# Performance work log

Hardware: AMD Instinct MI355X
Metric: run time of the kernel (lower is better)

Reference implementation:

```python
import jax, jax.numpy as jnp
import numpy as np

D_MODEL = 768
N_HEADS_CFG = 12
D_STATE = 32
D_CONV = 4
EXPAND = 2
HEADDIM = D_MODEL // N_HEADS_CFG          # 64
D_INNER = EXPAND * D_MODEL                # 1536
NHEADS = D_INNER // HEADDIM               # 24 (Mamba2 internal heads)
CONV_DIM = D_INNER + 2 * D_STATE          # 1600
D_IN_PROJ = 2 * D_INNER + 2 * D_STATE + NHEADS  # 3160
EPS = 1e-5
B_SZ, SEQ = 2, 512


def rmsnorm(x, w):
    return x * jax.lax.rsqrt(jnp.mean(x * x, axis=-1, keepdims=True) + EPS) * w


def mamba2(u, Wi, cw, cb, dtb, Alog, Dp, nw, Wo):
    """Mamba2 mixer: in_proj -> causal depthwise conv(silu) -> selective scan -> gated RMSNorm -> out_proj."""
    b, l, _ = u.shape
    zxbcdt = u @ Wi.T                                   # [b,l,d_in_proj]
    z, xBC, dt = jnp.split(zxbcdt, [D_INNER, D_INNER + CONV_DIM], axis=-1)
    # causal depthwise conv over time
    xBC = jnp.transpose(xBC, (0, 2, 1))                 # [b,c,l]
    xBC = jax.lax.conv_general_dilated(
        xBC, cw[:, None, :], window_strides=(1,),
        padding=[(D_CONV - 1, 0)], feature_group_count=CONV_DIM)
    xBC = jax.nn.silu(jnp.transpose(xBC + cb[None, :, None], (0, 2, 1)))
    x, Bm, Cm = jnp.split(xBC, [D_INNER, D_INNER + D_STATE], axis=-1)
    x = x.reshape(b, l, NHEADS, HEADDIM)                # [b,l,h,p]
    dt = jax.nn.softplus(dt + dtb)                      # [b,l,h]
    A = -jnp.exp(Alog)                                  # [h]
    a = jnp.exp(dt * A)                                 # decay [b,l,h]
    # dt * x outer B  -> [b,l,h,p,n]
    dBx = (dt[..., None, None] * x[..., None]) * Bm[:, :, None, None, :]

    def combine(e1, e2):
        a1, h1 = e1
        a2, h2 = e2
        return (a1 * a2, a2[..., None, None] * h1 + h2)

    _, h = jax.lax.associative_scan(combine, (a, dBx), axis=1)  # h: [b,l,h,p,n]
    y = jnp.einsum('blhpn,bln->blhp', h, Cm) + Dp[None, None, :, None] * x
    y = y.reshape(b, l, D_INNER)
    y = rmsnorm(y * jax.nn.silu(z), nw)                 # gated RMSNorm
    return y @ Wo.T                                     # [b,l,d_model]


def _mamba_params(key, scale=0.02):
    ks = jax.random.split(key, 6)
    return dict(
        in_w=jax.random.normal(ks[0], (D_IN_PROJ, D_MODEL), jnp.float32) * scale,
        conv_w=jax.random.normal(ks[1], (CONV_DIM, D_CONV), jnp.float32) * scale,
        conv_b=jnp.zeros((CONV_DIM,), jnp.float32),
        dt_bias=jax.random.uniform(ks[2], (NHEADS,), jnp.float32, -4.0, -1.0),
        A_log=jnp.log(jax.random.uniform(ks[3], (NHEADS,), jnp.float32, 1.0, 16.0)),
        D=jnp.ones((NHEADS,), jnp.float32),
        norm_w=jnp.ones((D_INNER,), jnp.float32),
        out_w=jax.random.normal(ks[4], (D_MODEL, D_INNER), jnp.float32) * scale,
    )


def setup_inputs() -> dict:
    key = jax.random.key(0)
    kx, kf, kb, ko = jax.random.split(key, 4)
    f = _mamba_params(kf)
    bw = _mamba_params(kb)
    return {
        'x': jax.random.normal(kx, (B_SZ, SEQ, D_MODEL), jnp.float32),
        'norm_w': jnp.ones((D_MODEL,), jnp.float32),
        'fwd_in_w': f['in_w'], 'fwd_conv_w': f['conv_w'], 'fwd_conv_b': f['conv_b'],
        'fwd_dt_bias': f['dt_bias'], 'fwd_A_log': f['A_log'], 'fwd_D': f['D'],
        'fwd_norm_w': f['norm_w'], 'fwd_out_w': f['out_w'],
        'bwd_in_w': bw['in_w'], 'bwd_conv_w': bw['conv_w'], 'bwd_conv_b': bw['conv_b'],
        'bwd_dt_bias': bw['dt_bias'], 'bwd_A_log': bw['A_log'], 'bwd_D': bw['D'],
        'bwd_norm_w': bw['norm_w'], 'bwd_out_w': bw['out_w'],
        'out_proj_w': jax.random.normal(ko, (D_MODEL, 2 * D_MODEL), jnp.float32) * 0.02,
    }


def reference(x, norm_w,
              fwd_in_w, fwd_conv_w, fwd_conv_b, fwd_dt_bias, fwd_A_log, fwd_D, fwd_norm_w, fwd_out_w,
              bwd_in_w, bwd_conv_w, bwd_conv_b, bwd_dt_bias, bwd_A_log, bwd_D, bwd_norm_w, bwd_out_w,
              out_proj_w):
    h = rmsnorm(x, norm_w)
    f_out = mamba2(h, fwd_in_w, fwd_conv_w, fwd_conv_b, fwd_dt_bias, fwd_A_log, fwd_D, fwd_norm_w, fwd_out_w)
    b_out = mamba2(h[:, ::-1], bwd_in_w, bwd_conv_w, bwd_conv_b, bwd_dt_bias, bwd_A_log, bwd_D, bwd_norm_w, bwd_out_w)[:, ::-1]
    return x + jnp.concatenate([f_out, b_out], axis=-1) @ out_proj_w.T
```

## Files before the change

kernel.cpp:

```cpp
#include <hip/hip_runtime.h>
#include <hip/hip_bf16.h>

#define DMODEL 768
#define DINNER 1536
#define DSTATE 32
#define NHEADS 24
#define HEADDIM 64
#define CONVDIM 1600
#define DINPROJ 3160
#define NPAD 3200
#define SEQ 512
#define MROWS 1024
#define CL 64
#define NCH 8

typedef __attribute__((ext_vector_type(8))) short bf16x8;
typedef __attribute__((ext_vector_type(4))) float f32x4;

__device__ __forceinline__ ushort f2bs(float v) {
  __hip_bfloat16 b = __float2bfloat16(v);
  return __builtin_bit_cast(unsigned short, b);
}

__device__ __forceinline__ void gld16(const void* g, const void* l) {
  __builtin_amdgcn_global_load_lds((const __attribute__((address_space(1))) void*)g,
                                   (__attribute__((address_space(3))) void*)l, 16, 0, 0);
}

__device__ __forceinline__ float block_reduce_sum(float v, float* ws4) {
#pragma unroll
  for (int o = 32; o > 0; o >>= 1) v += __shfl_xor(v, o, 64);
  int wid = threadIdx.x >> 6;
  if ((threadIdx.x & 63) == 0) ws4[wid] = v;
  __syncthreads();
  return ws4[0] + ws4[1] + ws4[2] + ws4[3];
}

__global__ __launch_bounds__(256) void prep_kernel(
    const float* __restrict__ x, const float* __restrict__ w, ushort* __restrict__ h,
    const float* __restrict__ s0, const float* __restrict__ s1,
    const float* __restrict__ s2, const float* __restrict__ s3,
    const float* __restrict__ s4, ushort* __restrict__ d) {
  if (blockIdx.x < MROWS) {
    __shared__ float ws4[4];
    int m = blockIdx.x;
    const float* xr = x + (size_t)m * DMODEL;
    float v[3];
    float ss = 0.f;
#pragma unroll
    for (int i = 0; i < 3; ++i) {
      v[i] = xr[threadIdx.x + i * 256];
      ss += v[i] * v[i];
    }
    ss = block_reduce_sum(ss, ws4);
    float sc = rsqrtf(ss / (float)DMODEL + 1e-5f);
    ushort* hr = h + (size_t)m * DMODEL;
#pragma unroll
    for (int i = 0; i < 3; ++i) {
      int c = threadIdx.x + i * 256;
      hr[c] = f2bs(v[i] * sc * w[c]);
    }
    return;
  }
  constexpr size_t NP_IN = (size_t)NPAD * DMODEL;
  constexpr size_t NE_IN = (size_t)DINPROJ * DMODEL;
  constexpr size_t NE_O = (size_t)DMODEL * DINNER;
  size_t i = (((size_t)blockIdx.x - MROWS) * 256 + threadIdx.x) * 4;
  const float* src;
  size_t off, ne;
  if (i < NP_IN) { src = s0; off = i; ne = NE_IN; }
  else if (i < 2 * NP_IN) { src = s1; off = i - NP_IN; ne = NE_IN; }
  else if (i < 2 * NP_IN + NE_O) { src = s2; off = i - 2 * NP_IN; ne = NE_O; }
  else if (i < 2 * NP_IN + 2 * NE_O) { src = s3; off = i - 2 * NP_IN - NE_O; ne = NE_O; }
  else if (i < 2 * NP_IN + 3 * NE_O) { src = s4; off = i - 2 * NP_IN - 2 * NE_O; ne = NE_O; }
  else return;
  ushort* dp = d + i;
  if (off + 3 < ne) {
    float4 v = *(const float4*)(src + off);
    dp[0] = f2bs(v.x); dp[1] = f2bs(v.y); dp[2] = f2bs(v.z); dp[3] = f2bs(v.w);
  } else {
#pragma unroll
    for (int j = 0; j < 4; ++j) dp[j] = (off + j < ne) ? f2bs(src[off + j]) : (ushort)0;
  }
}

template <int BM, int BN, bool ADD_X, bool OUT_BF16>
__global__ __launch_bounds__(256) void gemm4(
    const ushort* __restrict__ A, int lda, size_t aZ,
    const ushort* __restrict__ Bw, int ldb, size_t bZ,
    void* __restrict__ Cout, int ldc, size_t cZ,
    const float* __restrict__ X, int ldx, int K) {
  constexpr int AG = BM / 16;
  constexpr int BG = BN / 16;
  constexpr int MR = BM / 32;
  constexpr int NR = BN / 32;
  __shared__ ushort As[2][BM * 32];
  __shared__ ushort Bs[2][BN * 32];
  const int t = threadIdx.x, w = t >> 6, l = t & 63;
  int bx, by;
  {
    int gx = gridDim.x, gy = gridDim.y;
    int nwg = gx * gy;
    int flat = blockIdx.y * gx + blockIdx.x;
    int s = (flat & 7) * (nwg >> 3) + (flat >> 3);
    bx = s / gy; by = s % gy;
  }
  const int m0 = by * BM, n0 = bx * BN;
  const int wr = w >> 1, wc = w & 1;
  const int fr = l & 15, fq = l >> 4;
  const int sr = l >> 2, sc2 = (l & 3) * 8;
  const ushort* Ap = A + (size_t)blockIdx.z * aZ;
  const ushort* Bp = Bw + (size_t)blockIdx.z * bZ;

  auto stage = [&](int bb, int k0) {
#pragma unroll
    for (int g = w; g < AG + BG; g += 4) {
      if (g < AG)
        gld16(Ap + (size_t)(m0 + g * 16 + sr) * lda + k0 + sc2, (const char*)&As[bb][0] + g * 1024);
      else
        gld16(Bp + (size_t)(n0 + (g - AG) * 16 + sr) * ldb + k0 + sc2,
              (const char*)&Bs[bb][0] + (g - AG) * 1024);
    }
  };

  f32x4 acc[MR][NR];
#pragma unroll
  for (int m = 0; m < MR; ++m)
#pragma unroll
    for (int n = 0; n < NR; ++n) acc[m][n] = (f32x4){0.f, 0.f, 0.f, 0.f};

  stage(0, 0);
  __syncthreads();
  int cur = 0;
  const int nk = K / 32;
  for (int k = 0; k < nk; ++k) {
    if (k + 1 < nk) stage(cur ^ 1, (k + 1) * 32);
    bf16x8 af[MR], bfr[NR];
#pragma unroll
    for (int m = 0; m < MR; ++m)
      af[m] = *(const bf16x8*)&As[cur][(wr * (BM / 2) + m * 16 + fr) * 32 + fq * 8];
#pragma unroll
    for (int n = 0; n < NR; ++n)
      bfr[n] = *(const bf16x8*)&Bs[cur][(wc * (BN / 2) + n * 16 + fr) * 32 + fq * 8];
#pragma unroll
    for (int m = 0; m < MR; ++m)
#pragma unroll
      for (int n = 0; n < NR; ++n)
        acc[m][n] = __builtin_amdgcn_mfma_f32_16x16x32_bf16(af[m], bfr[n], acc[m][n], 0, 0, 0);
    __syncthreads();
    cur ^= 1;
  }

#pragma unroll
  for (int m = 0; m < MR; ++m) {
#pragma unroll
    for (int n = 0; n < NR; ++n) {
      int col = n0 + wc * (BN / 2) + n * 16 + fr;
#pragma unroll
      for (int j = 0; j < 4; ++j) {
        int row = m0 + wr * (BM / 2) + m * 16 + fq * 4 + j;
        float v = acc[m][n][j];
        if (ADD_X) v += X[(size_t)row * ldx + col];
        if (OUT_BF16)
          ((ushort*)Cout + (size_t)blockIdx.z * cZ)[(size_t)row * ldc + col] = f2bs(v);
        else
          ((float*)Cout + (size_t)blockIdx.z * cZ)[(size_t)row * ldc + col] = v;
      }
    }
  }
}

__global__ __launch_bounds__(256) void conv_dt_kernel(
    const float* __restrict__ zx,
    const float* __restrict__ cw0, const float* __restrict__ cb0,
    const float* __restrict__ dtb0, const float* __restrict__ Al0,
    const float* __restrict__ cw1, const float* __restrict__ cb1,
    const float* __restrict__ dtb1, const float* __restrict__ Al1,
    float* __restrict__ xbc, float* __restrict__ dta) {
  int m = blockIdx.x;
  int dir = blockIdx.y;
  int l = m & (SEQ - 1);
  const float* cw = dir ? cw1 : cw0;
  const float* cb = dir ? cb1 : cb0;
  const float* zrow = zx + (size_t)m * 6400 + dir * 3200 + DINNER;
  float* xo = xbc + ((size_t)dir * MROWS + m) * CONVDIM;
  for (int c = threadIdx.x; c < CONVDIM; c += 256) {
    float acc = cb[c];
    if (dir == 0) {
#pragma unroll
      for (int d = 0; d < 4; ++d) {
        if (l - d >= 0) acc = fmaf(zrow[-(size_t)d * 6400 + c], cw[c * 4 + 3 - d], acc);
      }
    } else {
#pragma unroll
      for (int d = 0; d < 4; ++d) {
        if (l + d < SEQ) acc = fmaf(zrow[(size_t)d * 6400 + c], cw[c * 4 + 3 - d], acc);
      }
    }
    xo[c] = acc / (1.f + expf(-acc));
  }
  if (threadIdx.x < NHEADS) {
    int hh = threadIdx.x;
    const float* dtb = dir ? dtb1 : dtb0;
    const float* Al = dir ? Al1 : Al0;
    float v = zx[(size_t)m * 6400 + dir * 3200 + DINNER + CONVDIM + hh] + dtb[hh];
    float dt = (v > 20.f) ? v : log1pf(expf(v));
    float A = -expf(Al[hh]);
    dta[((size_t)dir * MROWS + m) * 48 + hh] = dt;
    dta[((size_t)dir * MROWS + m) * 48 + NHEADS + hh] = expf(dt * A);
  }
}

__global__ __launch_bounds__(256) void scan_phase1(
    const float* __restrict__ xbc, const float* __restrict__ dta,
    float* __restrict__ sbuf, float* __restrict__ abuf) {
  __shared__ float xs[CL][64];
  __shared__ float bcs[CL][64];
  __shared__ float das[CL][2];
  int c = blockIdx.x, bh = blockIdx.y, dir = blockIdx.z;
  int b = bh / NHEADS, h = bh % NHEADS;
  int t = threadIdx.x, p = t >> 2, q = t & 3;
  const float* xb = xbc + ((size_t)dir * MROWS + b * SEQ) * CONVDIM;
  int lrow = t >> 4, lcol = (t & 15) * 4;
#pragma unroll
  for (int r = 0; r < 4; ++r) {
    int s = r * 16 + lrow;
    int tau = c * CL + s;
    int prow = dir ? (SEQ - 1 - tau) : tau;
    const float* rowp = xb + (size_t)prow * CONVDIM;
    *(float4*)&xs[s][lcol] = *(const float4*)(rowp + h * HEADDIM + lcol);
    *(float4*)&bcs[s][lcol] = *(const float4*)(rowp + DINNER + lcol);
  }
  if (t < 128) {
    int s = t >> 1, wsel = t & 1;
    int tau = c * CL + s;
    int prow = dir ? (SEQ - 1 - tau) : tau;
    das[s][wsel] = dta[((size_t)dir * MROWS + b * SEQ + prow) * 48 + wsel * NHEADS + h];
  }
  __syncthreads();
  float hst[8];
#pragma unroll
  for (int j = 0; j < 8; ++j) hst[j] = 0.f;
  float alpha = 1.f;
#pragma unroll 8
  for (int s = 0; s < CL; ++s) {
    float xp = xs[s][p];
    float dt_s = das[s][0], a_s = das[s][1];
    float cx = dt_s * xp;
    alpha *= a_s;
    float4 B0 = *(const float4*)&bcs[s][q * 8];
    float4 B1 = *(const float4*)&bcs[s][q * 8 + 4];
    float Bv[8] = {B0.x, B0.y, B0.z, B0.w, B1.x, B1.y, B1.z, B1.w};
#pragma unroll
    for (int j = 0; j < 8; ++j) hst[j] = fmaf(a_s, hst[j], cx * Bv[j]);
  }
  float* sp = sbuf + (((size_t)(dir * 48 + bh)) * NCH + c) * 2048 + p * 32 + q * 8;
  *(float4*)sp = (float4){hst[0], hst[1], hst[2], hst[3]};
  *(float4*)(sp + 4) = (float4){hst[4], hst[5], hst[6], hst[7]};
  if (t == 0) abuf[(dir * 48 + bh) * NCH + c] = alpha;
}

__global__ __launch_bounds__(256) void scan_phase3b(
    const float* __restrict__ xbc, const float* __restrict__ dta,
    const float* __restrict__ sbuf, const float* __restrict__ abuf,
    const float* __restrict__ Dp0, const float* __restrict__ Dp1,
    float* __restrict__ y) {
  __shared__ float xs[CL][64];
  __shared__ float bcs[CL][64];
  __shared__ float das[CL][2];
  int c = blockIdx.x, bh = blockIdx.y, dir = blockIdx.z;
  int b = bh / NHEADS, h = bh % NHEADS;
  int t = threadIdx.x, p = t >> 2, q = t & 3;
  const float* xb = xbc + ((size_t)dir * MROWS + b * SEQ) * CONVDIM;
  int lrow = t >> 4, lcol = (t & 15) * 4;
#pragma unroll
  for (int r = 0; r < 4; ++r) {
    int s = r * 16 + lrow;
    int tau = c * CL + s;
    int prow = dir ? (SEQ - 1 - tau) : tau;
    const float* rowp = xb + (size_t)prow * CONVDIM;
    *(float4*)&xs[s][lcol] = *(const float4*)(rowp + h * HEADDIM + lcol);
    *(float4*)&bcs[s][lcol] = *(const float4*)(rowp + DINNER + lcol);
  }
  if (t < 128) {
    int s = t >> 1, wsel = t & 1;
    int tau = c * CL + s;
    int prow = dir ? (SEQ - 1 - tau) : tau;
    das[s][wsel] = dta[((size_t)dir * MROWS + b * SEQ + prow) * 48 + wsel * NHEADS + h];
  }

  float hst[8];
#pragma unroll
  for (int j = 0; j < 8; ++j) hst[j] = 0.f;
  for (int cc = 0; cc < c; ++cc) {
    const float* sp = sbuf + (((size_t)(dir * 48 + bh)) * NCH + cc) * 2048 + p * 32 + q * 8;
    float4 s0 = *(const float4*)sp;
    float4 s1 = *(const float4*)(sp + 4);
    float al = abuf[(dir * 48 + bh) * NCH + cc];
    float sv[8] = {s0.x, s0.y, s0.z, s0.w, s1.x, s1.y, s1.z, s1.w};
#pragma unroll
    for (int j = 0; j < 8; ++j) hst[j] = fmaf(al, hst[j], sv[j]);
  }

  float Dv = (dir ? Dp1 : Dp0)[h];
  __syncthreads();
#pragma unroll 8
  for (int s = 0; s < CL; ++s) {
    float xp = xs[s][p];
    float dt_s = das[s][0], a_s = das[s][1];
    float cx = dt_s * xp;
    float4 B0 = *(const float4*)&bcs[s][q * 8];
    float4 B1 = *(const float4*)&bcs[s][q * 8 + 4];
    float4 C0 = *(const float4*)&bcs[s][32 + q * 8];
    float4 C1 = *(const float4*)&bcs[s][32 + q * 8 + 4];
    float Bv[8] = {B0.x, B0.y, B0.z, B0.w, B1.x, B1.y, B1.z, B1.w};
    float Cv[8] = {C0.x, C0.y, C0.z, C0.w, C1.x, C1.y, C1.z, C1.w};
    float acc = 0.f;
#pragma unroll
    for (int j = 0; j < 8; ++j) {
      hst[j] = fmaf(a_s, hst[j], cx * Bv[j]);
      acc = fmaf(hst[j], Cv[j], acc);
    }
    acc += __shfl_xor(acc, 1, 64);
    acc += __shfl_xor(acc, 2, 64);
    if (q == 0) {
      int tau = c * CL + s;
      int prow = dir ? (SEQ - 1 - tau) : tau;
      y[((size_t)dir * MROWS + b * SEQ + prow) * DINNER + h * HEADDIM + p] = fmaf(Dv, xp, acc);
    }
  }
}

__global__ __launch_bounds__(256) void gated_norm_kernel(
    const float* __restrict__ y,
    const float* __restrict__ zx,
    const float* __restrict__ nw0, const float* __restrict__ nw1,
    ushort* __restrict__ yn) {
  __shared__ float ws4[4];
  int m = blockIdx.x;
  int dir = blockIdx.y;
  const float* nw = dir ? nw1 : nw0;
  float g[6];
  float ss = 0.f;
#pragma unroll
  for (int i = 0; i < 6; ++i) {
    int c = threadIdx.x + i * 256;
    float yv = y[((size_t)dir * MROWS + m) * DINNER + c];
    float zv = zx[(size_t)m * 6400 + dir * 3200 + c];
    float gg = yv * (zv / (1.f + expf(-zv)));
    g[i] = gg;
    ss += gg * gg;
  }
  ss = block_reduce_sum(ss, ws4);
  float sc = rsqrtf(ss / (float)DINNER + 1e-5f);
#pragma unroll
  for (int i = 0; i < 6; ++i) {
    int c = threadIdx.x + i * 256;
    yn[((size_t)dir * MROWS + m) * DINNER + c] = f2bs(g[i] * sc * nw[c]);
  }
}

extern "C" void kernel_launch(void* const* d_in, const int* in_sizes, int n_in,
                              void* d_out, int out_size, void* d_ws, size_t ws_size,
                              hipStream_t stream) {
  const float* x = (const float*)d_in[0];
  const float* norm_w = (const float*)d_in[1];
  const float* in_w[2] = {(const float*)d_in[2], (const float*)d_in[10]};
  const float* conv_w[2] = {(const float*)d_in[3], (const float*)d_in[11]};
  const float* conv_b[2] = {(const float*)d_in[4], (const float*)d_in[12]};
  const float* dt_bias[2] = {(const float*)d_in[5], (const float*)d_in[13]};
  const float* A_log[2] = {(const float*)d_in[6], (const float*)d_in[14]};
  const float* Dp[2] = {(const float*)d_in[7], (const float*)d_in[15]};
  const float* nw[2] = {(const float*)d_in[8], (const float*)d_in[16]};
  const float* out_w[2] = {(const float*)d_in[9], (const float*)d_in[17]};
  const float* proj_w = (const float*)d_in[18];
  float* out = (float*)d_out;

  char* p = (char*)d_ws;
  float* zx = (float*)p;    p += (size_t)MROWS * 6400 * 4;
  float* xbc = (float*)p;   p += (size_t)2 * MROWS * CONVDIM * 4;
  float* dta = (float*)p;   p += (size_t)2 * MROWS * 48 * 4;
  float* y = (float*)p;     p += (size_t)2 * MROWS * DINNER * 4;
  float* sbuf = (float*)p;  p += (size_t)96 * NCH * 2048 * 4;
  float* abuf = (float*)p;  p += (size_t)96 * NCH * 4;
  ushort* h = (ushort*)p;   p += (size_t)MROWS * DMODEL * 2;
  ushort* yn = (ushort*)p;  p += (size_t)2 * MROWS * DINNER * 2;
  ushort* cat = (ushort*)p; p += (size_t)MROWS * DINNER * 2;
  ushort* wi = (ushort*)p;  p += (size_t)2 * NPAD * DMODEL * 2;
  ushort* wo = (ushort*)p;  p += (size_t)2 * DMODEL * DINNER * 2;
  ushort* wp = (ushort*)p;  p += (size_t)DMODEL * DINNER * 2;

  {
    size_t tot = 2 * (size_t)NPAD * DMODEL + 3 * (size_t)DMODEL * DINNER;
    int fblocks = (int)((tot / 4 + 255) / 256);
    prep_kernel<<<MROWS + fblocks, 256, 0, stream>>>(x, norm_w, h, in_w[0], in_w[1],
                                                     out_w[0], out_w[1], proj_w, wi);
  }

  {
    dim3 g(6400 / 128, MROWS / 64, 1);
    gemm4<64, 128, false, false><<<g, 256, 0, stream>>>(h, DMODEL, 0, wi, DMODEL, 0,
                                                        zx, 6400, 0, nullptr, 0, DMODEL);
  }

  conv_dt_kernel<<<dim3(MROWS, 2), 256, 0, stream>>>(
      zx, conv_w[0], conv_b[0], dt_bias[0], A_log[0],
      conv_w[1], conv_b[1], dt_bias[1], A_log[1], xbc, dta);

  scan_phase1<<<dim3(NCH, 48, 2), 256, 0, stream>>>(xbc, dta, sbuf, abuf);
  scan_phase3b<<<dim3(NCH, 48, 2), 256, 0, stream>>>(xbc, dta, sbuf, abuf, Dp[0], Dp[1], y);

  gated_norm_kernel<<<dim3(MROWS, 2), 256, 0, stream>>>(y, zx, nw[0], nw[1], yn);

  {
    dim3 g(DMODEL / 64, MROWS / 64, 2);
    gemm4<64, 64, false, true><<<g, 256, 0, stream>>>(
        yn, DINNER, (size_t)MROWS * DINNER, wo, DINNER, (size_t)DMODEL * DINNER,
        cat, DINNER, (size_t)DMODEL, nullptr, 0, DINNER);
  }

  {
    dim3 g(DMODEL / 64, MROWS / 64, 1);
    gemm4<64, 64, true, false><<<g, 256, 0, stream>>>(cat, DINNER, 0, wp, DINNER, 0,
                                                      out, DMODEL, 0, x, DMODEL, DINNER);
  }
}
```

Baseline: 128.6 us.

## Store intermediates as bf16 and triple-buffer GEMM loads with explicit vmcnt waits

The in-projection output (zx) and the conv output (xbc) are now stored as bf16 instead of fp32, which halves global traffic for the GEMM epilogue, the conv, the scan staging and the gated norm. Consumers unpack bf16 to fp32 on load. Separately, the GEMM changes from double to triple buffering, using global_load_lds prefetch two tiles ahead with explicit s_waitcnt vmcnt counts and raw s_barrier in place of __syncthreads. This adds bf16 rounding error on intermediates and increases LDS per block, which may lower occupancy.

```diff
diff --git a/kernel.cpp b/kernel.cpp
--- a/kernel.cpp
+++ b/kernel.cpp
@@ -21,10 +21,23 @@
   __hip_bfloat16 b = __float2bfloat16(v);
   return __builtin_bit_cast(unsigned short, b);
 }
+__device__ __forceinline__ float b2f(ushort u) {
+  return __uint_as_float(((uint)u) << 16);
+}
 
 __device__ __forceinline__ void gld16(const void* g, const void* l) {
   __builtin_amdgcn_global_load_lds((const __attribute__((address_space(1))) void*)g,
                                    (__attribute__((address_space(3))) void*)l, 16, 0, 0);
+}
+
+__device__ __forceinline__ void wait_vm(int n) {
+  switch (n) {
+    case 0: asm volatile("s_waitcnt vmcnt(0)" ::: "memory"); break;
+    case 2: asm volatile("s_waitcnt vmcnt(2)" ::: "memory"); break;
+    case 3: asm volatile("s_waitcnt vmcnt(3)" ::: "memory"); break;
+    case 4: asm volatile("s_waitcnt vmcnt(4)" ::: "memory"); break;
+    default: asm volatile("s_waitcnt vmcnt(6)" ::: "memory"); break;
+  }
 }
 
 __device__ __forceinline__ float block_reduce_sum(float v, float* ws4) {
@@ -85,17 +98,18 @@
 }
 
 template <int BM, int BN, bool ADD_X, bool OUT_BF16>
-__global__ __launch_bounds__(256) void gemm4(
+__global__ __launch_bounds__(256) void gemm5(
     const ushort* __restrict__ A, int lda, size_t aZ,
     const ushort* __restrict__ Bw, int ldb, size_t bZ,
     void* __restrict__ Cout, int ldc, size_t cZ,
     const float* __restrict__ X, int ldx, int K) {
   constexpr int AG = BM / 16;
   constexpr int BG = BN / 16;
+  constexpr int LPT = (AG + BG) / 4;
   constexpr int MR = BM / 32;
   constexpr int NR = BN / 32;
-  __shared__ ushort As[2][BM * 32];
-  __shared__ ushort Bs[2][BN * 32];
+  __shared__ ushort As[3][BM * 32];
+  __shared__ ushort Bs[3][BN * 32];
   const int t = threadIdx.x, w = t >> 6, l = t & 63;
   int bx, by;
   {
@@ -129,26 +143,33 @@
 #pragma unroll
     for (int n = 0; n < NR; ++n) acc[m][n] = (f32x4){0.f, 0.f, 0.f, 0.f};
 
+  const int nk = K / 32;
   stage(0, 0);
-  __syncthreads();
-  int cur = 0;
-  const int nk = K / 32;
+  stage(1, 32);
+  stage(2, 64);
+  int b = 0;
   for (int k = 0; k < nk; ++k) {
-    if (k + 1 < nk) stage(cur ^ 1, (k + 1) * 32);
+    int rem = nk - 1 - k;
+    wait_vm(LPT * (rem < 2 ? rem : 2));
+    __builtin_amdgcn_sched_barrier(0);
+    __builtin_amdgcn_s_barrier();
+    __builtin_amdgcn_sched_barrier(0);
     bf16x8 af[MR], bfr[NR];
 #pragma unroll
     for (int m = 0; m < MR; ++m)
-      af[m] = *(const bf16x8*)&As[cur][(wr * (BM / 2) + m * 16 + fr) * 32 + fq * 8];
+      af[m] = *(const bf16x8*)&As[b][(wr * (BM / 2) + m * 16 + fr) * 32 + fq * 8];
 #pragma unroll
     for (int n = 0; n < NR; ++n)
-      bfr[n] = *(const bf16x8*)&Bs[cur][(wc * (BN / 2) + n * 16 + fr) * 32 + fq * 8];
+      bfr[n] = *(const bf16x8*)&Bs[b][(wc * (BN / 2) + n * 16 + fr) * 32 + fq * 8];
 #pragma unroll
     for (int m = 0; m < MR; ++m)
 #pragma unroll
       for (int n = 0; n < NR; ++n)
         acc[m][n] = __builtin_amdgcn_mfma_f32_16x16x32_bf16(af[m], bfr[n], acc[m][n], 0, 0, 0);
-    __syncthreads();
-    cur ^= 1;
+    __builtin_amdgcn_sched_barrier(0);
+    __builtin_amdgcn_s_barrier();
+    if (k + 3 < nk) stage(b, (k + 3) * 32);
+    b = (b == 2) ? 0 : b + 1;
   }
 
 #pragma unroll
@@ -171,39 +192,39 @@
 }
 
 __global__ __launch_bounds__(256) void conv_dt_kernel(
-    const float* __restrict__ zx,
+    const ushort* __restrict__ zxb,
     const float* __restrict__ cw0, const float* __restrict__ cb0,
     const float* __restrict__ dtb0, const float* __restrict__ Al0,
     const float* __restrict__ cw1, const float* __restrict__ cb1,
     const float* __restrict__ dtb1, const float* __restrict__ Al1,
-    float* __restrict__ xbc, float* __restrict__ dta) {
+    ushort* __restrict__ xbc, float* __restrict__ dta) {
   int m = blockIdx.x;
   int dir = blockIdx.y;
   int l = m & (SEQ - 1);
   const float* cw = dir ? cw1 : cw0;
   const float* cb = dir ? cb1 : cb0;
-  const float* zrow = zx + (size_t)m * 6400 + dir * 3200 + DINNER;
-  float* xo = xbc + ((size_t)dir * MROWS + m) * CONVDIM;
+  const ushort* zrow = zxb + (size_t)m * 6400 + dir * 3200 + DINNER;
+  ushort* xo = xbc + ((size_t)dir * MROWS + m) * CONVDIM;
   for (int c = threadIdx.x; c < CONVDIM; c += 256) {
     float acc = cb[c];
     if (dir == 0) {
 #pragma unroll
       for (int d = 0; d < 4; ++d) {
-        if (l - d >= 0) acc = fmaf(zrow[-(size_t)d * 6400 + c], cw[c * 4 + 3 - d], acc);
+        if (l - d >= 0) acc = fmaf(b2f(zrow[-(ptrdiff_t)d * 6400 + c]), cw[c * 4 + 3 - d], acc);
       }
     } else {
 #pragma unroll
       for (int d = 0; d < 4; ++d) {
-        if (l + d < SEQ) acc = fmaf(zrow[(size_t)d * 6400 + c], cw[c * 4 + 3 - d], acc);
+        if (l + d < SEQ) acc = fmaf(b2f(zrow[(ptrdiff_t)d * 6400 + c]), cw[c * 4 + 3 - d], acc);
       }
     }
-    xo[c] = acc / (1.f + expf(-acc));
+    xo[c] = f2bs(acc / (1.f + expf(-acc)));
   }
   if (threadIdx.x < NHEADS) {
     int hh = threadIdx.x;
     const float* dtb = dir ? dtb1 : dtb0;
     const float* Al = dir ? Al1 : Al0;
-    float v = zx[(size_t)m * 6400 + dir * 3200 + DINNER + CONVDIM + hh] + dtb[hh];
+    float v = b2f(zxb[(size_t)m * 6400 + dir * 3200 + DINNER + CONVDIM + hh]) + dtb[hh];
     float dt = (v > 20.f) ? v : log1pf(expf(v));
     float A = -expf(Al[hh]);
     dta[((size_t)dir * MROWS + m) * 48 + hh] = dt;
@@ -211,8 +232,29 @@
   }
 }
 
+__device__ __forceinline__ void scan_stage(
+    const ushort* __restrict__ xb, int c, int dir, int h, int t,
+    float xs[CL][64], float bcs[CL][64]) {
+#pragma unroll
+  for (int i = 0; i < 4; ++i) {
+    int slot = t + i * 256;
+    int s = slot >> 4, seg = (slot >> 3) & 1, o8 = slot & 7;
+    int tau = c * CL + s;
+    int prow = dir ? (SEQ - 1 - tau) : tau;
+    const ushort* rp = xb + (size_t)prow * CONVDIM + (seg ? DINNER : h * HEADDIM) + o8 * 8;
+    uint4 u = *(const uint4*)rp;
+    float* dst = seg ? &bcs[s][o8 * 8] : &xs[s][o8 * 8];
+    uint ua[4] = {u.x, u.y, u.z, u.w};
+#pragma unroll
+    for (int j = 0; j < 4; ++j) {
+      dst[j * 2] = __uint_as_float((ua[j] & 0xffffu) << 16);
+      dst[j * 2 + 1] = __uint_as_float(ua[j] & 0xffff0000u);
+    }
+  }
+}
+
 __global__ __launch_bounds__(256) void scan_phase1(
-    const float* __restrict__ xbc, const float* __restrict__ dta,
+    const ushort* __restrict__ xbc, const float* __restrict__ dta,
     float* __restrict__ sbuf, float* __restrict__ abuf) {
   __shared__ float xs[CL][64];
   __shared__ float bcs[CL][64];
@@ -220,17 +262,8 @@
   int c = blockIdx.x, bh = blockIdx.y, dir = blockIdx.z;
   int b = bh / NHEADS, h = bh % NHEADS;
   int t = threadIdx.x, p = t >> 2, q = t & 3;
-  const float* xb = xbc + ((size_t)dir * MROWS + b * SEQ) * CONVDIM;
-  int lrow = t >> 4, lcol = (t & 15) * 4;
-#pragma unroll
-  for (int r = 0; r < 4; ++r) {
-    int s = r * 16 + lrow;
-    int tau = c * CL + s;
-    int prow = dir ? (SEQ - 1 - tau) : tau;
-    const float* rowp = xb + (size_t)prow * CONVDIM;
-    *(float4*)&xs[s][lcol] = *(const float4*)(rowp + h * HEADDIM + lcol);
-    *(float4*)&bcs[s][lcol] = *(const float4*)(rowp + DINNER + lcol);
-  }
+  const ushort* xb = xbc + ((size_t)dir * MROWS + b * SEQ) * CONVDIM;
+  scan_stage(xb, c, dir, h, t, xs, bcs);
   if (t < 128) {
     int s = t >> 1, wsel = t & 1;
     int tau = c * CL + s;
@@ -261,7 +294,7 @@
 }
 
 __global__ __launch_bounds__(256) void scan_phase3b(
-    const float* __restrict__ xbc, const float* __restrict__ dta,
+    const ushort* __restrict__ xbc, const float* __restrict__ dta,
     const float* __restrict__ sbuf, const float* __restrict__ abuf,
     const float* __restrict__ Dp0, const float* __restrict__ Dp1,
     float* __restrict__ y) {
@@ -271,17 +304,8 @@
   int c = blockIdx.x, bh = blockIdx.y, dir = blockIdx.z;
   int b = bh / NHEADS, h = bh % NHEADS;
   int t = threadIdx.x, p = t >> 2, q = t & 3;
-  const float* xb = xbc + ((size_t)dir * MROWS + b * SEQ) * CONVDIM;
-  int lrow = t >> 4, lcol = (t & 15) * 4;
-#pragma unroll
-  for (int r = 0; r < 4; ++r) {
-    int s = r * 16 + lrow;
-    int tau = c * CL + s;
-    int prow = dir ? (SEQ - 1 - tau) : tau;
-    const float* rowp = xb + (size_t)prow * CONVDIM;
-    *(float4*)&xs[s][lcol] = *(const float4*)(rowp + h * HEADDIM + lcol);
-    *(float4*)&bcs[s][lcol] = *(const float4*)(rowp + DINNER + lcol);
-  }
+  const ushort* xb = xbc + ((size_t)dir * MROWS + b * SEQ) * CONVDIM;
+  scan_stage(xb, c, dir, h, t, xs, bcs);
   if (t < 128) {
     int s = t >> 1, wsel = t & 1;
     int tau = c * CL + s;
@@ -333,7 +357,7 @@
 
 __global__ __launch_bounds__(256) void gated_norm_kernel(
     const float* __restrict__ y,
-    const float* __restrict__ zx,
+    const ushort* __restrict__ zxb,
     const float* __restrict__ nw0, const float* __restrict__ nw1,
     ushort* __restrict__ yn) {
   __shared__ float ws4[4];
@@ -346,7 +370,7 @@
   for (int i = 0; i < 6; ++i) {
     int c = threadIdx.x + i * 256;
     float yv = y[((size_t)dir * MROWS + m) * DINNER + c];
-    float zv = zx[(size_t)m * 6400 + dir * 3200 + c];
+    float zv = b2f(zxb[(size_t)m * 6400 + dir * 3200 + c]);
     float gg = yv * (zv / (1.f + expf(-zv)));
     g[i] = gg;
     ss += gg * gg;
@@ -377,8 +401,8 @@
   float* out = (float*)d_out;
 
   char* p = (char*)d_ws;
-  float* zx = (float*)p;    p += (size_t)MROWS * 6400 * 4;
-  float* xbc = (float*)p;   p += (size_t)2 * MROWS * CONVDIM * 4;
+  ushort* zxb = (ushort*)p; p += (size_t)MROWS * 6400 * 2;
+  ushort* xbc = (ushort*)p; p += (size_t)2 * MROWS * CONVDIM * 2;
   float* dta = (float*)p;   p += (size_t)2 * MROWS * 48 * 4;
   float* y = (float*)p;     p += (size_t)2 * MROWS * DINNER * 4;
   float* sbuf = (float*)p;  p += (size_t)96 * NCH * 2048 * 4;
@@ -399,29 +423,29 @@
 
   {
     dim3 g(6400 / 128, MROWS / 64, 1);
-    gemm4<64, 128, false, false><<<g, 256, 0, stream>>>(h, DMODEL, 0, wi, DMODEL, 0,
-                                                        zx, 6400, 0, nullptr, 0, DMODEL);
+    gemm5<64, 128, false, true><<<g, 256, 0, stream>>>(h, DMODEL, 0, wi, DMODEL, 0,
+                                                       zxb, 6400, 0, nullptr, 0, DMODEL);
   }
 
   conv_dt_kernel<<<dim3(MROWS, 2), 256, 0, stream>>>(
-      zx, conv_w[0], conv_b[0], dt_bias[0], A_log[0],
+      zxb, conv_w[0], conv_b[0], dt_bias[0], A_log[0],
       conv_w[1], conv_b[1], dt_bias[1], A_log[1], xbc, dta);
 
   scan_phase1<<<dim3(NCH, 48, 2), 256, 0, stream>>>(xbc, dta, sbuf, abuf);
   scan_phase3b<<<dim3(NCH, 48, 2), 256, 0, stream>>>(xbc, dta, sbuf, abuf, Dp[0], Dp[1], y);
 
-  gated_norm_kernel<<<dim3(MROWS, 2), 256, 0, stream>>>(y, zx, nw[0], nw[1], yn);
+  gated_norm_kernel<<<dim3(MROWS, 2), 256, 0, stream>>>(y, zxb, nw[0], nw[1], yn);
 
   {
     dim3 g(DMODEL / 64, MROWS / 64, 2);
-    gemm4<64, 64, false, true><<<g, 256, 0, stream>>>(
+    gemm5<64, 64, false, true><<<g, 256, 0, stream>>>(
         yn, DINNER, (size_t)MROWS * DINNER, wo, DINNER, (size_t)DMODEL * DINNER,
         cat, DINNER, (size_t)DMODEL, nullptr, 0, DINNER);
   }
 
   {
     dim3 g(DMODEL / 64, MROWS / 64, 1);
-    gemm4<64, 64, true, false><<<g, 256, 0, stream>>>(cat, DINNER, 0, wp, DINNER, 0,
+    gemm5<64, 64, true, false><<<g, 256, 0, stream>>>(cat, DINNER, 0, wp, DINNER, 0,
                                                       out, DMODEL, 0, x, DMODEL, DINNER);
   }
 }
```

New measurement: 125.2 us. 1.03x faster.
